# Performance work log

Measured on AMD Instinct MI355X. Metric: run time of the kernel, lower is better.

Reference implementation:

```python
import jax, jax.numpy as jnp
import numpy as np

B, F, D = 1024, 160000, 16


def setup_inputs() -> dict:
    key = jax.random.key(0)
    k1, k2, k3 = jax.random.split(key, 3)
    x = jax.random.randint(k1, (B, F), 0, 2, dtype=jnp.int32)  # multi-hot transaction
    emb_w = jax.random.normal(k2, (F, D), dtype=jnp.float32) * 0.05  # FM factor table
    bias_w = jax.random.normal(k3, (F, 1), dtype=jnp.float32) * 0.05  # per-field linear bias
    g_bias = jnp.zeros((), dtype=jnp.float32)  # global bias
    return {"x": x, "emb_w": emb_w, "bias_w": bias_w, "g_bias": g_bias}


def reference(x, emb_w, bias_w, g_bias):
    # mask[b,f] = 1 where field f is active (row > 0 in original tf code)
    mask = (x > 0).astype(emb_w.dtype)  # [B, F]
    # sum of active embeddings per row: equals gather+sum in the original
    ev = mask @ emb_w  # [B, D]
    # sum of squared norms of active embeddings per row
    rowsq = jnp.sum(emb_w * emb_w, axis=1)  # [F]
    sum_sq = mask @ rowsq  # [B]
    # 0.5 * (sum_{i,j} e_i . e_j - sum_i ||e_i||^2) == FM pairwise interaction
    second = 0.5 * (jnp.sum(ev * ev, axis=-1) - sum_sq)  # [B]
    # linear term: global bias + sum of active field biases
    linear = g_bias + mask @ bias_w  # [B, 1]
    return linear + second[:, None]  # [B, 1]
```

## Files before the change

kernel.cpp:

```cpp
#include <hip/hip_runtime.h>
#include <hip/hip_bf16.h>

#define B_ROWS 1024
#define F_FLD  160000
#define D_DIM  16
#define NKB    (F_FLD / 32)
#define NSTAT  (D_DIM + 1)
#define ACC_N  (B_ROWS * NSTAT)
#define CCOLS  6400
#define NGRP   (CCOLS / 256)
#define KBC    (CCOLS / 32)
#define NCHUNK (F_FLD / CCOLS)
#define ROWS_B 32
#define ROWBLK (B_ROWS / ROWS_B)
#define WAVES  8

typedef __attribute__((ext_vector_type(8))) short bf16x8;
typedef __attribute__((ext_vector_type(4))) float f32x4;

static __device__ inline unsigned short f2bf(float x) {
    __hip_bfloat16 h = __float2bfloat16(x);
    union { __hip_bfloat16 h; unsigned short s; } u; u.h = h; return u.s;
}

static __device__ inline bf16x8 expand8(unsigned b) {
    union { unsigned u[4]; bf16x8 v; } r;
    r.u[0] = ((b        & 1u) * 0x3F80u) | (((b >> 1) & 1u) * 0x3F800000u);
    r.u[1] = (((b >> 2) & 1u) * 0x3F80u) | (((b >> 3) & 1u) * 0x3F800000u);
    r.u[2] = (((b >> 4) & 1u) * 0x3F80u) | (((b >> 5) & 1u) * 0x3F800000u);
    r.u[3] = (((b >> 6) & 1u) * 0x3F80u) | (((b >> 7) & 1u) * 0x3F800000u);
    return r.v;
}

__global__ __launch_bounds__(256) void fm_pack(const float* __restrict__ emb,
                                               const float* __restrict__ bias,
                                               unsigned short* __restrict__ embB,
                                               unsigned short* __restrict__ cB2c,
                                               float* __restrict__ acc) {
    const int tid = threadIdx.x;
    const int kb = blockIdx.x * 4 + (tid >> 6);
    const int l = tid & 63, q = l >> 4, n = l & 15;

    float e[8];
    union { unsigned short s[8]; uint4 u; } v;
#pragma unroll
    for (int j = 0; j < 8; ++j) {
        int f = kb * 32 + 4 * j + q;
        e[j] = emb[(size_t)f * D_DIM + n];
        v.s[j] = f2bf(e[j]);
    }
    *(uint4*)(embB + ((size_t)kb * 64 + l) * 8) = v.u;

    union { unsigned short s[8]; uint4 u; } w;
#pragma unroll
    for (int j = 0; j < 8; ++j) {
        float s = e[j] * e[j];
        s += __shfl_xor(s, 1);
        s += __shfl_xor(s, 2);
        s += __shfl_xor(s, 4);
        s += __shfl_xor(s, 8);
        int f = kb * 32 + 4 * j + q;
        w.s[j] = f2bf((n == 0 ? bias[f] : 0.0f) - 0.5f * s);
    }
    if (n == 0) *(uint4*)(cB2c + ((size_t)kb * 4 + q) * 8) = w.u;

    int gid = blockIdx.x * 256 + tid;
    if (gid < ACC_N) acc[gid] = 0.0f;
}

__global__ __launch_bounds__(512, 6) void fm_main(const int* __restrict__ x,
                                                  const unsigned short* __restrict__ embB,
                                                  const unsigned short* __restrict__ cB2c,
                                                  float* __restrict__ acc) {
    __shared__ unsigned long long msk[NGRP][ROWS_B][4];
    __shared__ float red[WAVES][ROWS_B][NSTAT];

    const int tid = threadIdx.x;
    const int w = tid >> 6, l = tid & 63;
    const int q = l >> 4, n = l & 15;
    const int rowbase = blockIdx.x * ROWS_B;
    const int c0 = blockIdx.y * CCOLS;

#pragma unroll
    for (int rr = 0; rr < 4; ++rr) {
        const int rloc = 4 * w + rr;
        const int4* xp = (const int4*)(x + (size_t)(rowbase + rloc) * F_FLD + c0) + l;
        for (int g0 = 0; g0 < NGRP; g0 += 5) {
            int4 v[5];
#pragma unroll
            for (int k = 0; k < 5; ++k) v[k] = xp[(size_t)(g0 + k) * 64];
#pragma unroll
            for (int k = 0; k < 5; ++k) {
                unsigned long long m0 = __ballot(v[k].x > 0);
                unsigned long long m1 = __ballot(v[k].y > 0);
                unsigned long long m2 = __ballot(v[k].z > 0);
                unsigned long long m3 = __ballot(v[k].w > 0);
                if (l == 0) {
                    msk[g0 + k][rloc][0] = m0; msk[g0 + k][rloc][1] = m1;
                    msk[g0 + k][rloc][2] = m2; msk[g0 + k][rloc][3] = m3;
                }
            }
        }
    }
    __syncthreads();

    f32x4 aev0 = {0.f, 0.f, 0.f, 0.f}, ac0 = {0.f, 0.f, 0.f, 0.f};
    f32x4 aev1 = {0.f, 0.f, 0.f, 0.f}, ac1 = {0.f, 0.f, 0.f, 0.f};
    const uint4* eB = (const uint4*)embB;
    const uint4* cB = (const uint4*)cB2c;
    const int kbg0 = blockIdx.y * KBC;

#pragma unroll 2
    for (int t = 0; t < KBC / WAVES; ++t) {
        const int kb = w * (KBC / WAVES) + t;
        const int g = kb >> 3, byt = kb & 7;
        unsigned long long mv0 = msk[g][n][q];
        unsigned long long mv1 = msk[g][n + 16][q];
        unsigned b0 = (unsigned)(mv0 >> (8 * byt)) & 0xFFu;
        unsigned b1 = (unsigned)(mv1 >> (8 * byt)) & 0xFFu;
        bf16x8 A0 = expand8(b0);
        bf16x8 A1 = expand8(b1);
        union { uint4 u; bf16x8 v; } Bf, Cf;
        Bf.u = eB[(size_t)(kbg0 + kb) * 64 + l];
        Cf.u = cB[(size_t)(kbg0 + kb) * 4 + q];
        aev0 = __builtin_amdgcn_mfma_f32_16x16x32_bf16(A0, Bf.v, aev0, 0, 0, 0);
        ac0  = __builtin_amdgcn_mfma_f32_16x16x32_bf16(A0, Cf.v, ac0,  0, 0, 0);
        aev1 = __builtin_amdgcn_mfma_f32_16x16x32_bf16(A1, Bf.v, aev1, 0, 0, 0);
        ac1  = __builtin_amdgcn_mfma_f32_16x16x32_bf16(A1, Cf.v, ac1,  0, 0, 0);
    }

#pragma unroll
    for (int r = 0; r < 4; ++r) {
        red[w][q * 4 + r][n] = aev0[r];
        red[w][16 + q * 4 + r][n] = aev1[r];
        if (n == 0) {
            red[w][q * 4 + r][16] = ac0[r];
            red[w][16 + q * 4 + r][16] = ac1[r];
        }
    }
    __syncthreads();

    for (int i = tid; i < ROWS_B * NSTAT; i += 512) {
        int row = i / NSTAT, col = i % NSTAT;
        float s = 0.0f;
#pragma unroll
        for (int ww = 0; ww < WAVES; ++ww) s += red[ww][row][col];
        atomicAdd(acc + (size_t)(rowbase + row) * NSTAT + col, s);
    }
}

__global__ __launch_bounds__(256) void fm_final(const float* __restrict__ acc,
                                                const float* __restrict__ g_bias,
                                                float* __restrict__ out) {
    int row = blockIdx.x * 256 + threadIdx.x;
    if (row >= B_ROWS) return;
    const float* a = acc + (size_t)row * NSTAT;
    float s = 0.0f;
#pragma unroll
    for (int d = 0; d < D_DIM; ++d) s += a[d] * a[d];
    out[row] = g_bias[0] + a[16] + 0.5f * s;
}

extern "C" void kernel_launch(void* const* d_in, const int* in_sizes, int n_in,
                              void* d_out, int out_size, void* d_ws, size_t ws_size,
                              hipStream_t stream) {
    const int*   x      = (const int*)d_in[0];
    const float* emb_w  = (const float*)d_in[1];
    const float* bias_w = (const float*)d_in[2];
    const float* g_bias = (const float*)d_in[3];
    float*       out    = (float*)d_out;

    unsigned short* embB = (unsigned short*)d_ws;
    unsigned short* cB2c = (unsigned short*)((char*)d_ws + (size_t)NKB * 64 * 8 * 2);
    float*          acc  = (float*)((char*)d_ws + (size_t)NKB * 64 * 8 * 2
                                                + (size_t)NKB * 4 * 8 * 2);

    fm_pack<<<dim3(NKB / 4), dim3(256), 0, stream>>>(emb_w, bias_w, embB, cB2c, acc);
    fm_main<<<dim3(ROWBLK, NCHUNK), dim3(512), 0, stream>>>(x, embB, cB2c, acc);
    fm_final<<<dim3((B_ROWS + 255) / 256), dim3(256), 0, stream>>>(acc, g_bias, out);
}
```

Before: 850.7 us.

## Move x bitmask packing into prep kernel alongside embedding packing

The ballot-based compression of the int32 multi-hot matrix into bitmasks moves out of the MFMA kernel into a separate prep pass. That pass runs in the same launch as the embedding bf16 packing, with one wave per row streaming the whole row and double-buffering its loads. The main kernel then loads compact precomputed bitmasks into shared memory, laid out row-major, instead of streaming 655MB of x itself. This separates the bandwidth-bound scan from the compute phase at the cost of an extra global bitmask write and read, and the prep grid has only 256 row blocks (1024 waves), which may limit memory parallelism.

```diff
diff --git a/kernel.cpp b/kernel.cpp
--- a/kernel.cpp
+++ b/kernel.cpp
@@ -9,11 +9,14 @@
 #define ACC_N  (B_ROWS * NSTAT)
 #define CCOLS  6400
 #define NGRP   (CCOLS / 256)
+#define NGRP_T (F_FLD / 256)
 #define KBC    (CCOLS / 32)
 #define NCHUNK (F_FLD / CCOLS)
 #define ROWS_B 32
 #define ROWBLK (B_ROWS / ROWS_B)
 #define WAVES  8
+#define PREBLK 256
+#define PACKBLK (NKB / 4)
 
 typedef __attribute__((ext_vector_type(8))) short bf16x8;
 typedef __attribute__((ext_vector_type(4))) float f32x4;
@@ -32,74 +35,96 @@
     return r.v;
 }
 
-__global__ __launch_bounds__(256) void fm_pack(const float* __restrict__ emb,
+__global__ __launch_bounds__(256) void fm_prep(const int* __restrict__ x,
+                                               const float* __restrict__ emb,
                                                const float* __restrict__ bias,
+                                               unsigned long long* __restrict__ bm,
                                                unsigned short* __restrict__ embB,
                                                unsigned short* __restrict__ cB2c,
                                                float* __restrict__ acc) {
     const int tid = threadIdx.x;
-    const int kb = blockIdx.x * 4 + (tid >> 6);
-    const int l = tid & 63, q = l >> 4, n = l & 15;
-
-    float e[8];
-    union { unsigned short s[8]; uint4 u; } v;
-#pragma unroll
-    for (int j = 0; j < 8; ++j) {
-        int f = kb * 32 + 4 * j + q;
-        e[j] = emb[(size_t)f * D_DIM + n];
-        v.s[j] = f2bf(e[j]);
-    }
-    *(uint4*)(embB + ((size_t)kb * 64 + l) * 8) = v.u;
-
-    union { unsigned short s[8]; uint4 u; } w;
-#pragma unroll
-    for (int j = 0; j < 8; ++j) {
-        float s = e[j] * e[j];
-        s += __shfl_xor(s, 1);
-        s += __shfl_xor(s, 2);
-        s += __shfl_xor(s, 4);
-        s += __shfl_xor(s, 8);
-        int f = kb * 32 + 4 * j + q;
-        w.s[j] = f2bf((n == 0 ? bias[f] : 0.0f) - 0.5f * s);
-    }
-    if (n == 0) *(uint4*)(cB2c + ((size_t)kb * 4 + q) * 8) = w.u;
-
-    int gid = blockIdx.x * 256 + tid;
-    if (gid < ACC_N) acc[gid] = 0.0f;
-}
-
-__global__ __launch_bounds__(512, 6) void fm_main(const int* __restrict__ x,
+    if (blockIdx.x < PREBLK) {
+        const int w = tid >> 6, l = tid & 63;
+        const int row = blockIdx.x * 4 + w;
+        const int4* xp = (const int4*)(x + (size_t)row * F_FLD) + l;
+        unsigned long long* dst = bm + (size_t)row * NGRP_T * 4;
+
+        int4 va[5], vb[5];
+#pragma unroll
+        for (int k = 0; k < 5; ++k) va[k] = xp[(size_t)k * 64];
+        for (int g0 = 0; g0 < NGRP_T; g0 += 5) {
+            const int nx = g0 + 5;
+            if (nx < NGRP_T) {
+#pragma unroll
+                for (int k = 0; k < 5; ++k) vb[k] = xp[(size_t)(nx + k) * 64];
+            }
+#pragma unroll
+            for (int k = 0; k < 5; ++k) {
+                unsigned long long m0 = __ballot(va[k].x > 0);
+                unsigned long long m1 = __ballot(va[k].y > 0);
+                unsigned long long m2 = __ballot(va[k].z > 0);
+                unsigned long long m3 = __ballot(va[k].w > 0);
+                unsigned long long mv = (l == 1) ? m1 : (l == 2) ? m2 : (l == 3) ? m3 : m0;
+                if (l < 4) dst[(size_t)(g0 + k) * 4 + l] = mv;
+            }
+            if (nx < NGRP_T) {
+#pragma unroll
+                for (int k = 0; k < 5; ++k) va[k] = vb[k];
+            }
+        }
+    } else {
+        const int bid = blockIdx.x - PREBLK;
+        const int kb = bid * 4 + (tid >> 6);
+        const int l = tid & 63, q = l >> 4, n = l & 15;
+
+        float e[8];
+        union { unsigned short s[8]; uint4 u; } v;
+#pragma unroll
+        for (int j = 0; j < 8; ++j) {
+            int f = kb * 32 + 4 * j + q;
+            e[j] = emb[(size_t)f * D_DIM + n];
+            v.s[j] = f2bf(e[j]);
+        }
+        *(uint4*)(embB + ((size_t)kb * 64 + l) * 8) = v.u;
+
+        union { unsigned short s[8]; uint4 u; } wv;
+#pragma unroll
+        for (int j = 0; j < 8; ++j) {
+            float s = e[j] * e[j];
+            s += __shfl_xor(s, 1);
+            s += __shfl_xor(s, 2);
+            s += __shfl_xor(s, 4);
+            s += __shfl_xor(s, 8);
+            int f = kb * 32 + 4 * j + q;
+            wv.s[j] = f2bf((n == 0 ? bias[f] : 0.0f) - 0.5f * s);
+        }
+        if (n == 0) *(uint4*)(cB2c + ((size_t)kb * 4 + q) * 8) = wv.u;
+
+        int gid = bid * 256 + tid;
+        if (gid < ACC_N) acc[gid] = 0.0f;
+    }
+}
+
+__global__ __launch_bounds__(512, 6) void fm_main(const unsigned long long* __restrict__ bm,
                                                   const unsigned short* __restrict__ embB,
                                                   const unsigned short* __restrict__ cB2c,
                                                   float* __restrict__ acc) {
-    __shared__ unsigned long long msk[NGRP][ROWS_B][4];
+    __shared__ unsigned long long msk[ROWS_B][NGRP][4];
     __shared__ float red[WAVES][ROWS_B][NSTAT];
 
     const int tid = threadIdx.x;
     const int w = tid >> 6, l = tid & 63;
     const int q = l >> 4, n = l & 15;
     const int rowbase = blockIdx.x * ROWS_B;
-    const int c0 = blockIdx.y * CCOLS;
+    const int ch = blockIdx.y;
 
 #pragma unroll
     for (int rr = 0; rr < 4; ++rr) {
         const int rloc = 4 * w + rr;
-        const int4* xp = (const int4*)(x + (size_t)(rowbase + rloc) * F_FLD + c0) + l;
-        for (int g0 = 0; g0 < NGRP; g0 += 5) {
-            int4 v[5];
-#pragma unroll
-            for (int k = 0; k < 5; ++k) v[k] = xp[(size_t)(g0 + k) * 64];
-#pragma unroll
-            for (int k = 0; k < 5; ++k) {
-                unsigned long long m0 = __ballot(v[k].x > 0);
-                unsigned long long m1 = __ballot(v[k].y > 0);
-                unsigned long long m2 = __ballot(v[k].z > 0);
-                unsigned long long m3 = __ballot(v[k].w > 0);
-                if (l == 0) {
-                    msk[g0 + k][rloc][0] = m0; msk[g0 + k][rloc][1] = m1;
-                    msk[g0 + k][rloc][2] = m2; msk[g0 + k][rloc][3] = m3;
-                }
-            }
+        const uint4* src = (const uint4*)(bm + ((size_t)(rowbase + rloc) * NGRP_T
+                                                + (size_t)ch * NGRP) * 4);
+        if (l < NGRP * 2) {
+            ((uint4*)&msk[rloc][0][0])[l] = src[l];
         }
     }
     __syncthreads();
@@ -114,8 +139,8 @@
     for (int t = 0; t < KBC / WAVES; ++t) {
         const int kb = w * (KBC / WAVES) + t;
         const int g = kb >> 3, byt = kb & 7;
-        unsigned long long mv0 = msk[g][n][q];
-        unsigned long long mv1 = msk[g][n + 16][q];
+        unsigned long long mv0 = msk[n][g][q];
+        unsigned long long mv1 = msk[n + 16][g][q];
         unsigned b0 = (unsigned)(mv0 >> (8 * byt)) & 0xFFu;
         unsigned b1 = (unsigned)(mv1 >> (8 * byt)) & 0xFFu;
         bf16x8 A0 = expand8(b0);
@@ -174,8 +199,13 @@
     unsigned short* cB2c = (unsigned short*)((char*)d_ws + (size_t)NKB * 64 * 8 * 2);
     float*          acc  = (float*)((char*)d_ws + (size_t)NKB * 64 * 8 * 2
                                                 + (size_t)NKB * 4 * 8 * 2);
-
-    fm_pack<<<dim3(NKB / 4), dim3(256), 0, stream>>>(emb_w, bias_w, embB, cB2c, acc);
-    fm_main<<<dim3(ROWBLK, NCHUNK), dim3(512), 0, stream>>>(x, embB, cB2c, acc);
+    unsigned long long* bm = (unsigned long long*)((char*)d_ws
+                                                + (size_t)NKB * 64 * 8 * 2
+                                                + (size_t)NKB * 4 * 8 * 2
+                                                + (size_t)ACC_N * 4);
+
+    fm_prep<<<dim3(PREBLK + PACKBLK), dim3(256), 0, stream>>>(x, emb_w, bias_w,
+                                                              bm, embB, cB2c, acc);
+    fm_main<<<dim3(ROWBLK, NCHUNK), dim3(512), 0, stream>>>(bm, embB, cB2c, acc);
     fm_final<<<dim3((B_ROWS + 255) / 256), dim3(256), 0, stream>>>(acc, g_bias, out);
 }
```

After: 916.8 us. 7.8% more time.

## Pre-pack input mask into bitmaps in a separate streaming pass fused with weight pack

Applied to the files above, without the earlier changes.

Adds a prep stage that streams the int32 input matrix once with many waves and software double-buffered loads, compressing it to a 4-bit-per-int4 bitmap in workspace. The weight packing runs in the same launch on extra blocks. The main MFMA kernel then reads the compact bitmap instead of the raw input, so its load phase shrinks. This trades an extra global write and read of the bitmap and a dependency between stages for a better-parallelised streaming read of the dominant input.

```diff
diff --git a/kernel.cpp b/kernel.cpp
--- a/kernel.cpp
+++ b/kernel.cpp
@@ -7,13 +7,21 @@
 #define NKB    (F_FLD / 32)
 #define NSTAT  (D_DIM + 1)
 #define ACC_N  (B_ROWS * NSTAT)
+#define SEGC   1280
+#define NSEG   (F_FLD / SEGC)
 #define CCOLS  6400
 #define NGRP   (CCOLS / 256)
+#define SEGB   (CCOLS / SEGC)
 #define KBC    (CCOLS / 32)
 #define NCHUNK (F_FLD / CCOLS)
 #define ROWS_B 32
 #define ROWBLK (B_ROWS / ROWS_B)
 #define WAVES  8
+#define SBLK   2000
+#define SWAVES (SBLK * 4)
+#define UNITS  (B_ROWS * NSEG)
+#define UPW    (UNITS / SWAVES)
+#define PACKBLK (NKB / 4)
 
 typedef __attribute__((ext_vector_type(8))) short bf16x8;
 typedef __attribute__((ext_vector_type(4))) float f32x4;
@@ -32,43 +40,78 @@
     return r.v;
 }
 
-__global__ __launch_bounds__(256) void fm_pack(const float* __restrict__ emb,
+__global__ __launch_bounds__(256) void fm_prep(const int* __restrict__ x,
+                                               const float* __restrict__ emb,
                                                const float* __restrict__ bias,
+                                               unsigned* __restrict__ bm2,
                                                unsigned short* __restrict__ embB,
                                                unsigned short* __restrict__ cB2c,
                                                float* __restrict__ acc) {
     const int tid = threadIdx.x;
-    const int kb = blockIdx.x * 4 + (tid >> 6);
-    const int l = tid & 63, q = l >> 4, n = l & 15;
-
-    float e[8];
-    union { unsigned short s[8]; uint4 u; } v;
-#pragma unroll
-    for (int j = 0; j < 8; ++j) {
-        int f = kb * 32 + 4 * j + q;
-        e[j] = emb[(size_t)f * D_DIM + n];
-        v.s[j] = f2bf(e[j]);
-    }
-    *(uint4*)(embB + ((size_t)kb * 64 + l) * 8) = v.u;
-
-    union { unsigned short s[8]; uint4 u; } w;
-#pragma unroll
-    for (int j = 0; j < 8; ++j) {
-        float s = e[j] * e[j];
-        s += __shfl_xor(s, 1);
-        s += __shfl_xor(s, 2);
-        s += __shfl_xor(s, 4);
-        s += __shfl_xor(s, 8);
-        int f = kb * 32 + 4 * j + q;
-        w.s[j] = f2bf((n == 0 ? bias[f] : 0.0f) - 0.5f * s);
-    }
-    if (n == 0) *(uint4*)(cB2c + ((size_t)kb * 4 + q) * 8) = w.u;
-
-    int gid = blockIdx.x * 256 + tid;
-    if (gid < ACC_N) acc[gid] = 0.0f;
-}
-
-__global__ __launch_bounds__(512, 6) void fm_main(const int* __restrict__ x,
+    if (blockIdx.x < SBLK) {
+        const int gw = blockIdx.x * 4 + (tid >> 6);
+        const int l = tid & 63;
+        const int4* xb = (const int4*)x;
+
+        int4 a[5], b[5];
+        auto LD = [&](int4 (&r)[5], int u) {
+            const int4* p = xb + (size_t)u * (SEGC / 4) + l;
+#pragma unroll
+            for (int k = 0; k < 5; ++k) r[k] = p[(size_t)k * 64];
+        };
+        auto ST = [&](int4 (&r)[5], int u) {
+            unsigned m = 0;
+#pragma unroll
+            for (int k = 0; k < 5; ++k) {
+                unsigned nib = (unsigned)(r[k].x > 0) | ((unsigned)(r[k].y > 0) << 1)
+                             | ((unsigned)(r[k].z > 0) << 2) | ((unsigned)(r[k].w > 0) << 3);
+                m |= nib << (4 * k);
+            }
+            bm2[(size_t)u * 64 + l] = m;
+        };
+
+        LD(a, gw);
+#pragma unroll 1
+        for (int i = 0; i < UPW; i += 2) {
+            LD(b, gw + (i + 1) * SWAVES);
+            ST(a, gw + i * SWAVES);
+            if (i + 2 < UPW) LD(a, gw + (i + 2) * SWAVES);
+            ST(b, gw + (i + 1) * SWAVES);
+        }
+    } else {
+        const int bid = blockIdx.x - SBLK;
+        const int kb = bid * 4 + (tid >> 6);
+        const int l = tid & 63, q = l >> 4, n = l & 15;
+
+        float e[8];
+        union { unsigned short s[8]; uint4 u; } v;
+#pragma unroll
+        for (int j = 0; j < 8; ++j) {
+            int f = kb * 32 + 4 * j + q;
+            e[j] = emb[(size_t)f * D_DIM + n];
+            v.s[j] = f2bf(e[j]);
+        }
+        *(uint4*)(embB + ((size_t)kb * 64 + l) * 8) = v.u;
+
+        union { unsigned short s[8]; uint4 u; } wv;
+#pragma unroll
+        for (int j = 0; j < 8; ++j) {
+            float s = e[j] * e[j];
+            s += __shfl_xor(s, 1);
+            s += __shfl_xor(s, 2);
+            s += __shfl_xor(s, 4);
+            s += __shfl_xor(s, 8);
+            int f = kb * 32 + 4 * j + q;
+            wv.s[j] = f2bf((n == 0 ? bias[f] : 0.0f) - 0.5f * s);
+        }
+        if (n == 0) *(uint4*)(cB2c + ((size_t)kb * 4 + q) * 8) = wv.u;
+
+        int gid = bid * 256 + tid;
+        if (gid < ACC_N) acc[gid] = 0.0f;
+    }
+}
+
+__global__ __launch_bounds__(512, 6) void fm_main(const unsigned* __restrict__ bm2,
                                                   const unsigned short* __restrict__ embB,
                                                   const unsigned short* __restrict__ cB2c,
                                                   float* __restrict__ acc) {
@@ -79,25 +122,29 @@
     const int w = tid >> 6, l = tid & 63;
     const int q = l >> 4, n = l & 15;
     const int rowbase = blockIdx.x * ROWS_B;
-    const int c0 = blockIdx.y * CCOLS;
+    const int ch = blockIdx.y;
 
 #pragma unroll
     for (int rr = 0; rr < 4; ++rr) {
         const int rloc = 4 * w + rr;
-        const int4* xp = (const int4*)(x + (size_t)(rowbase + rloc) * F_FLD + c0) + l;
-        for (int g0 = 0; g0 < NGRP; g0 += 5) {
-            int4 v[5];
-#pragma unroll
-            for (int k = 0; k < 5; ++k) v[k] = xp[(size_t)(g0 + k) * 64];
-#pragma unroll
-            for (int k = 0; k < 5; ++k) {
-                unsigned long long m0 = __ballot(v[k].x > 0);
-                unsigned long long m1 = __ballot(v[k].y > 0);
-                unsigned long long m2 = __ballot(v[k].z > 0);
-                unsigned long long m3 = __ballot(v[k].w > 0);
+        const unsigned* src = bm2 + ((size_t)(rowbase + rloc) * NSEG
+                                     + (size_t)ch * SEGB) * 64 + l;
+        unsigned mreg[SEGB];
+#pragma unroll
+        for (int s = 0; s < SEGB; ++s) mreg[s] = src[(size_t)s * 64];
+#pragma unroll
+        for (int s = 0; s < SEGB; ++s) {
+            const unsigned m = mreg[s];
+#pragma unroll
+            for (int j = 0; j < 5; ++j) {
+                const int g = s * 5 + j;
+                unsigned long long b0 = __ballot((m >> (4 * j + 0)) & 1u);
+                unsigned long long b1 = __ballot((m >> (4 * j + 1)) & 1u);
+                unsigned long long b2 = __ballot((m >> (4 * j + 2)) & 1u);
+                unsigned long long b3 = __ballot((m >> (4 * j + 3)) & 1u);
                 if (l == 0) {
-                    msk[g0 + k][rloc][0] = m0; msk[g0 + k][rloc][1] = m1;
-                    msk[g0 + k][rloc][2] = m2; msk[g0 + k][rloc][3] = m3;
+                    msk[g][rloc][0] = b0; msk[g][rloc][1] = b1;
+                    msk[g][rloc][2] = b2; msk[g][rloc][3] = b3;
                 }
             }
         }
@@ -174,8 +221,12 @@
     unsigned short* cB2c = (unsigned short*)((char*)d_ws + (size_t)NKB * 64 * 8 * 2);
     float*          acc  = (float*)((char*)d_ws + (size_t)NKB * 64 * 8 * 2
                                                 + (size_t)NKB * 4 * 8 * 2);
-
-    fm_pack<<<dim3(NKB / 4), dim3(256), 0, stream>>>(emb_w, bias_w, embB, cB2c, acc);
-    fm_main<<<dim3(ROWBLK, NCHUNK), dim3(512), 0, stream>>>(x, embB, cB2c, acc);
+    unsigned*       bm2  = (unsigned*)((char*)d_ws + (size_t)NKB * 64 * 8 * 2
+                                                   + (size_t)NKB * 4 * 8 * 2
+                                                   + (size_t)ACC_N * 4);
+
+    fm_prep<<<dim3(SBLK + PACKBLK), dim3(256), 0, stream>>>(x, emb_w, bias_w,
+                                                            bm2, embB, cB2c, acc);
+    fm_main<<<dim3(ROWBLK, NCHUNK), dim3(512), 0, stream>>>(bm2, embB, cB2c, acc);
     fm_final<<<dim3((B_ROWS + 255) / 256), dim3(256), 0, stream>>>(acc, g_bias, out);
 }
```

Result: slower. 895.8 us (+5.3%).
